# Kernel tuning notes

Measured on AMD Instinct MI355X. Metric: run time of the kernel, lower is better.

## Reference

```python
import jax, jax.numpy as jnp
import numpy as np

N = 50000          # nodes
E = 800000         # edges (before self loops)
IC = 16            # in_channels; pos = x[:, :3]
H = (64, 64, 128, 128)
OUT = 8
INS = (IC, IC + H[0], IC + H[0] + H[1], IC + H[0] + H[1] + H[2])


def _lin_w(k, fi, fo):
    s = 1.0 / np.sqrt(fi)
    return jax.random.uniform(k, (fi, fo), minval=-s, maxval=s, dtype=jnp.float32)


def setup_inputs() -> dict:
    key = jax.random.key(0)
    ks = jax.random.split(key, 64)
    inp = {
        "x": jax.random.normal(ks[0], (N, IC), dtype=jnp.float32),
        "edge_index": jax.random.randint(ks[1], (2, E), 0, N, dtype=jnp.int32),
    }
    ki = 2
    for i, (fi, fo) in enumerate(zip(INS, H), start=1):
        inp[f"Wl{i}"] = _lin_w(ks[ki], fi, fo); ki += 1   # lin (values), no bias
        inp[f"Ws{i}"] = _lin_w(ks[ki], fi, fo); ki += 1   # lin_src, no bias
        inp[f"Wd{i}"] = _lin_w(ks[ki], fi, fo); ki += 1   # lin_dst, no bias
        inp[f"Wp{i}"] = _lin_w(ks[ki], 3, fo); ki += 1    # pos_nn = Linear(3, fo)
        inp[f"bp{i}"] = jnp.zeros((fo,), jnp.float32)
    inp["Wm1"] = _lin_w(ks[ki], IC + sum(H), 64); ki += 1
    inp["bm1"] = jnp.zeros((64,), jnp.float32)
    inp["Wm2"] = _lin_w(ks[ki], 64, OUT); ki += 1
    inp["bm2"] = jnp.zeros((OUT,), jnp.float32)
    return inp


def _pt_conv(h, pos, src, dst, Wl, Ws, Wd, Wp, bp, n):
    """PointTransformerConv: per-channel softmax attention over incoming edges."""
    a_src = h @ Ws                               # alpha_j part  [N, F]
    a_dst = h @ Wd                               # alpha_i part  [N, F]
    v = h @ Wl                                   # values        [N, F]
    delta = (pos[dst] - pos[src]) @ Wp + bp      # pos_nn(pos_i - pos_j)  [E, F]
    alpha = a_dst[dst] - a_src[src] + delta      # [E, F]
    m = jax.ops.segment_max(alpha, dst, num_segments=n)
    ea = jnp.exp(alpha - m[dst])
    s = jax.ops.segment_sum(ea, dst, num_segments=n)
    attn = ea / s[dst]                           # segment softmax (self loops -> s > 0)
    return jax.ops.segment_sum(attn * (v[src] + delta), dst, num_segments=n)


def reference(x, edge_index, Wl1, Ws1, Wd1, Wp1, bp1, Wl2, Ws2, Wd2, Wp2, bp2,
              Wl3, Ws3, Wd3, Wp3, bp3, Wl4, Ws4, Wd4, Wp4, bp4, Wm1, bm1, Wm2, bm2):
    n = x.shape[0]
    pos = x[:, :3]
    loop = jnp.arange(n, dtype=edge_index.dtype)
    src = jnp.concatenate([edge_index[0], loop])  # PyG add_self_loops (default True)
    dst = jnp.concatenate([edge_index[1], loop])
    lrelu = lambda v: jax.nn.leaky_relu(v, 0.01)
    x1 = lrelu(_pt_conv(x, pos, src, dst, Wl1, Ws1, Wd1, Wp1, bp1, n))
    h2 = jnp.concatenate([x, x1], 1)
    x2 = lrelu(_pt_conv(h2, pos, src, dst, Wl2, Ws2, Wd2, Wp2, bp2, n))
    h3 = jnp.concatenate([x, x1, x2], 1)
    x3 = lrelu(_pt_conv(h3, pos, src, dst, Wl3, Ws3, Wd3, Wp3, bp3, n))
    h4 = jnp.concatenate([x, x1, x2, x3], 1)
    x4 = lrelu(_pt_conv(h4, pos, src, dst, Wl4, Ws4, Wd4, Wp4, bp4, n))
    out = jnp.concatenate([x, x1, x2, x3, x4], 1)  # dropout = identity (eval mode)
    out = out @ Wm1 + bm1
    return out @ Wm2 + bm2
```

## Files before the change

kernel.cpp:

```cpp
#include <hip/hip_runtime.h>
#include <hip/hip_bf16.h>
#include <hip/hip_fp16.h>
#include <math.h>

#define N_NODES 50000
#define N_EDGES 800000
#define ET (N_EDGES + N_NODES)
#define HTOT 400

#define SCAN_CHUNK 1024
#define NSCB ((N_NODES + SCAN_CHUNK - 1) / SCAN_CHUNK)

typedef __attribute__((ext_vector_type(4))) float f32x4;
typedef __attribute__((ext_vector_type(8))) short bf16x8;

static const int INS_h[4] = {16, 80, 144, 272};
static const int K32_h[4] = {32, 96, 160, 288};
static const int HO_h[4]  = {64, 64, 128, 128};


__global__ void copy_x_kernel(const float* __restrict__ x, __hip_bfloat16* __restrict__ h) {
    int i = blockIdx.x * blockDim.x + threadIdx.x;
    if (i >= N_NODES * 16) return;
    int n = i >> 4, c = i & 15;
    h[n * HTOT + c] = __float2bfloat16(x[i]);
}

__global__ void hist_kernel(const int* __restrict__ ei, int* __restrict__ deg) {
    int e = blockIdx.x * blockDim.x + threadIdx.x;
    if (e >= ET) return;
    int dst = (e < N_EDGES) ? ei[N_EDGES + e] : (e - N_EDGES);
    atomicAdd(&deg[dst], 1);
}

__global__ __launch_bounds__(256) void scan_p1(const int* __restrict__ deg,
                                               int* __restrict__ bsum) {
    __shared__ int red[256];
    const int b = blockIdx.x, t = threadIdx.x;
    const int base = b * SCAN_CHUNK + t * 4;
    int s = 0;
#pragma unroll
    for (int j = 0; j < 4; ++j) {
        int i = base + j;
        if (i < N_NODES) s += deg[i];
    }
    red[t] = s;
    __syncthreads();
    for (int off = 128; off > 0; off >>= 1) {
        if (t < off) red[t] += red[t + off];
        __syncthreads();
    }
    if (t == 0) bsum[b] = red[0];
}

__global__ void scan_p2(int* __restrict__ bsum) {
    const int lane = threadIdx.x;
    int v = (lane < NSCB) ? bsum[lane] : 0;
    int inc = v;
#pragma unroll
    for (int off = 1; off < 64; off <<= 1) {
        int u = __shfl_up(inc, off);
        if (lane >= off) inc += u;
    }
    if (lane < NSCB) bsum[lane] = inc - v;
    if (lane == 63) bsum[NSCB] = inc;
}

__global__ __launch_bounds__(256) void scan_p3(const int* __restrict__ deg,
                                               const int* __restrict__ bsum,
                                               int* __restrict__ row_ptr,
                                               int* __restrict__ cursor) {
    __shared__ int ts[256];
    const int b = blockIdx.x, t = threadIdx.x;
    const int base = b * SCAN_CHUNK + t * 4;
    int v[4];
    int s = 0;
#pragma unroll
    for (int j = 0; j < 4; ++j) {
        int i = base + j;
        v[j] = (i < N_NODES) ? deg[i] : 0;
        s += v[j];
    }
    ts[t] = s;
    __syncthreads();
    for (int off = 1; off < 256; off <<= 1) {
        int u = (t >= off) ? ts[t - off] : 0;
        __syncthreads();
        ts[t] += u;
        __syncthreads();
    }
    int excl = bsum[b] + ts[t] - s;
#pragma unroll
    for (int j = 0; j < 4; ++j) {
        int i = base + j;
        if (i < N_NODES) {
            row_ptr[i] = excl;
            cursor[i] = excl;
            excl += v[j];
        }
    }
    if (b == 0 && t == 0) row_ptr[N_NODES] = bsum[NSCB];
}

__global__ void scatter_kernel(const int* __restrict__ ei, const float* __restrict__ x,
                               int* __restrict__ cursor, float4* __restrict__ edata) {
    int e = blockIdx.x * blockDim.x + threadIdx.x;
    if (e >= ET) return;
    int src, dst;
    if (e < N_EDGES) { src = ei[e]; dst = ei[N_EDGES + e]; }
    else             { src = dst = e - N_EDGES; }
    int p = atomicAdd(&cursor[dst], 1);
    float dx = x[dst * 16 + 0] - x[src * 16 + 0];
    float dy = x[dst * 16 + 1] - x[src * 16 + 1];
    float dz = x[dst * 16 + 2] - x[src * 16 + 2];
    edata[p] = make_float4(__int_as_float(src), dx, dy, dz);
}


__global__ void concat_wT_kernel(const float* __restrict__ W0, const float* __restrict__ W1,
                                 int K, int K32, int fo,
                                 __hip_bfloat16* __restrict__ Wt, int total) {
    int i = blockIdx.x * blockDim.x + threadIdx.x;
    if (i >= total) return;
    int c = i / K32, kk = i - c * K32;
    float v = 0.f;
    if (kk < K) {
        if (c < fo) v = W0[kk * fo + c];
        else        v = W1[kk * fo + (c - fo)];
    }
    Wt[i] = __float2bfloat16(v);
}


template <bool FUSE>
__global__ __launch_bounds__(256) void gemm3_kernel(
    const __hip_bfloat16* __restrict__ A, int lda,
    const __hip_bfloat16* __restrict__ Wt, int K32,
    const float* __restrict__ bias,
    __half* __restrict__ av, int fo,
    int M, int K,
    const float* __restrict__ W2, const float* __restrict__ b2,
    float* __restrict__ out) {
    __shared__ float smemf[9728];
    ushort* sA = (ushort*)smemf;
    ushort* sB = (ushort*)smemf + 10240;
    const int t = threadIdx.x;
    const int r0 = blockIdx.x * 128, c0 = blockIdx.y * 64;
    const int w = t >> 6, lane = t & 63;
    const int l15 = lane & 15, l4 = lane >> 4;

    f32x4 acc[2][4];
#pragma unroll
    for (int i = 0; i < 2; ++i)
#pragma unroll
        for (int j = 0; j < 4; ++j) acc[i][j] = (f32x4){0.f, 0.f, 0.f, 0.f};

    const int sr = t >> 2, sq = (t & 3) * 8;
    const int ar1 = min(r0 + sr, M - 1), ar2 = min(r0 + sr + 64, M - 1);
    const size_t a1b = (size_t)ar1 * lda, a2b = (size_t)ar2 * lda;
    const size_t wb = (size_t)(c0 + sr) * K32;
    const int nk = K32 >> 5;

    uint4 ga0, ga1, gb;
    const uint4 z4 = {0u, 0u, 0u, 0u};
    {
        const int kk = sq;
        const bool ok = kk < K;
        ga0 = ok ? *(const uint4*)(A + a1b + kk) : z4;
        ga1 = ok ? *(const uint4*)(A + a2b + kk) : z4;
        gb  = *(const uint4*)(Wt + wb + kk);
        *(uint4*)(sA + sr * 40 + sq) = ga0;
        *(uint4*)(sA + (sr + 64) * 40 + sq) = ga1;
        *(uint4*)(sB + sr * 40 + sq) = gb;
    }
    __syncthreads();

    int buf = 0;
    for (int kc = 0; kc < nk; ++kc) {
        const bool nx = (kc + 1) < nk;
        if (nx) {
            const int kk = (kc + 1) * 32 + sq;
            const bool ok = kk < K;
            ga0 = ok ? *(const uint4*)(A + a1b + kk) : z4;
            ga1 = ok ? *(const uint4*)(A + a2b + kk) : z4;
            gb  = *(const uint4*)(Wt + wb + kk);
        }
        const ushort* bA = sA + buf * 5120 + w * 1280;
        const ushort* bB = sB + buf * 2560;
        bf16x8 af[2], bfr[4];
#pragma unroll
        for (int i = 0; i < 2; ++i)
            af[i] = *(const bf16x8*)(bA + (i * 16 + l15) * 40 + l4 * 8);
#pragma unroll
        for (int j = 0; j < 4; ++j)
            bfr[j] = *(const bf16x8*)(bB + (j * 16 + l15) * 40 + l4 * 8);
#pragma unroll
        for (int i = 0; i < 2; ++i)
#pragma unroll
            for (int j = 0; j < 4; ++j)
                acc[i][j] = __builtin_amdgcn_mfma_f32_16x16x32_bf16(af[i], bfr[j], acc[i][j], 0, 0, 0);
        if (nx) {
            const int ob = buf ^ 1;
            *(uint4*)(sA + ob * 5120 + sr * 40 + sq) = ga0;
            *(uint4*)(sA + ob * 5120 + (sr + 64) * 40 + sq) = ga1;
            *(uint4*)(sB + ob * 2560 + sr * 40 + sq) = gb;
        }
        __syncthreads();
        buf ^= 1;
    }

    if (!FUSE) {
#pragma unroll
        for (int i = 0; i < 2; ++i)
#pragma unroll
            for (int j = 0; j < 4; ++j)
#pragma unroll
                for (int p = 0; p < 4; ++p) {
                    int row = r0 + w * 32 + i * 16 + l4 * 4 + p;
                    int col = c0 + j * 16 + l15;
                    if (row < M) {
                        int part = col >= fo;
                        int cc = col - part * fo;
                        av[((size_t)row * fo + cc) * 2 + part] = __float2half(acc[i][j][p]);
                    }
                }
    } else {
#pragma unroll
        for (int i = 0; i < 2; ++i)
#pragma unroll
            for (int j = 0; j < 4; ++j)
#pragma unroll
                for (int p = 0; p < 4; ++p) {
                    int lrow = w * 32 + i * 16 + l4 * 4 + p;
                    int col = j * 16 + l15;
                    smemf[lrow * 68 + col] = acc[i][j][p] + bias[col];
                }
        smemf[8704 + t] = W2[t];
        smemf[8704 + 256 + t] = W2[256 + t];
        __syncthreads();
        const int row = t >> 1, oc = (t & 1) * 4;
        f32x4 o = *(const f32x4*)&b2[oc];
#pragma unroll 8
        for (int k = 0; k < 64; ++k) {
            float a = smemf[row * 68 + k];
            o += a * *(const f32x4*)&smemf[8704 + k * 8 + oc];
        }
        const int grow = r0 + row;
        if (grow < M) *(f32x4*)&out[(size_t)grow * 8 + oc] = o;
    }
}


template <int CPL>
__global__ __launch_bounds__(256) void attn_kernel(
    __hip_bfloat16* __restrict__ h,
    const __half* __restrict__ av,
    const float* __restrict__ Wp, const float* __restrict__ bp,
    const int* __restrict__ rowp, const float4* __restrict__ edata,
    int colbase) {
    constexpr int FO = 16 * CPL;
    constexpr int NV = CPL / 4;
    const int wid = (blockIdx.x * (int)blockDim.x + (int)threadIdx.x) >> 6;
    if (wid >= N_NODES) return;
    const int lane = threadIdx.x & 63;
    const int e = lane >> 4, l16 = lane & 15;
    const int n = wid;
    const int cb = l16 * CPL;

    float wp0[CPL], wp1[CPL], wp2[CPL], bpv[CPL], s[CPL], num[CPL];
#pragma unroll
    for (int j = 0; j < CPL; ++j) {
        int c = cb + j;
        wp0[j] = Wp[c];
        wp1[j] = Wp[FO + c];
        wp2[j] = Wp[2 * FO + c];
        bpv[j] = bp[c];
        s[j] = 0.f; num[j] = 0.f;
    }
    const uint* av32 = (const uint*)av;
    const int beg = rowp[n], end = rowp[n + 1], last = end - 1;

    uint4 u[NV], un[NV];
    float4 ed, edn;
    {
        const int idx = min(beg + e, last);
        ed = edata[idx];
        const uint* rb = av32 + (size_t)__float_as_int(ed.x) * FO + cb;
#pragma unroll
        for (int q = 0; q < NV; ++q) u[q] = *(const uint4*)(rb + 4 * q);
    }
    for (int base = beg; base < end; base += 4) {
        const int nidx = min(base + 4 + e, last);
        edn = edata[nidx];
        const uint* rb = av32 + (size_t)__float_as_int(edn.x) * FO + cb;
#pragma unroll
        for (int q = 0; q < NV; ++q) un[q] = *(const uint4*)(rb + 4 * q);
        const bool val = (base + e) < end;
        const uint* up = (const uint*)u;
#pragma unroll
        for (int j = 0; j < CPL; ++j) {
            __half2 hv = *(const __half2*)&up[j];
            float as = __half2float(hv.x);
            float vv = __half2float(hv.y);
            float delta = fmaf(ed.y, wp0[j], fmaf(ed.z, wp1[j], fmaf(ed.w, wp2[j], bpv[j])));
            float p = val ? __expf(delta - as) : 0.f;
            s[j] += p;
            num[j] = fmaf(p, vv + delta, num[j]);
        }
        ed = edn;
#pragma unroll
        for (int q = 0; q < NV; ++q) u[q] = un[q];
    }
#pragma unroll
    for (int j = 0; j < CPL; ++j) {
        s[j] += __shfl_xor(s[j], 16);
        s[j] += __shfl_xor(s[j], 32);
        num[j] += __shfl_xor(num[j], 16);
        num[j] += __shfl_xor(num[j], 32);
    }
    if (e == 0) {
        ushort o[CPL];
#pragma unroll
        for (int j = 0; j < CPL; ++j) {
            float xi = num[j] / s[j];
            xi = xi > 0.f ? xi : 0.01f * xi;
            __hip_bfloat16 b = __float2bfloat16(xi);
            o[j] = *(ushort*)&b;
        }
        ushort* dst = (ushort*)&h[(size_t)n * HTOT + colbase + cb];
        if (CPL == 4)      *(uint2*)dst = *(uint2*)o;
        else               *(uint4*)dst = *(uint4*)o;
    }
}


extern "C" void kernel_launch(void* const* d_in, const int* in_sizes, int n_in,
                              void* d_out, int out_size, void* d_ws, size_t ws_size,
                              hipStream_t stream) {
    const float* x = (const float*)d_in[0];
    const int* ei = (const int*)d_in[1];
    const float *Wl[4], *Ws[4], *Wp[4], *bp[4];
    for (int i = 0; i < 4; ++i) {
        Wl[i] = (const float*)d_in[2 + 5 * i];
        Ws[i] = (const float*)d_in[3 + 5 * i];
        Wp[i] = (const float*)d_in[5 + 5 * i];
        bp[i] = (const float*)d_in[6 + 5 * i];
    }
    const float* Wm1 = (const float*)d_in[22];
    const float* bm1 = (const float*)d_in[23];
    const float* Wm2 = (const float*)d_in[24];
    const float* bm2 = (const float*)d_in[25];
    float* out = (float*)d_out;

    char* ws = (char*)d_ws;
    size_t off = 0;
    auto alloc = [&](size_t bytes) -> void* {
        void* p = ws + off;
        off += (bytes + 255) & ~(size_t)255;
        return p;
    };
    __hip_bfloat16* h = (__hip_bfloat16*)alloc((size_t)N_NODES * HTOT * 2);
    __half* av = (__half*)alloc((size_t)N_NODES * 256 * 2);
    __hip_bfloat16* Wt = (__hip_bfloat16*)alloc((size_t)384 * 416 * 2);
    int* deg = (int*)alloc((size_t)N_NODES * 4);
    int* rowp = (int*)alloc((size_t)(N_NODES + 1) * 4);
    int* cursor = (int*)alloc((size_t)N_NODES * 4);
    int* bsum = (int*)alloc((size_t)(NSCB + 1) * 4);
    float4* edata = (float4*)alloc((size_t)ET * 16);
    (void)ws_size; (void)n_in; (void)in_sizes; (void)out_size;

    hipMemsetAsync(deg, 0, (size_t)N_NODES * 4, stream);
    copy_x_kernel<<<(N_NODES * 16 + 255) / 256, 256, 0, stream>>>(x, h);
    hist_kernel<<<(ET + 255) / 256, 256, 0, stream>>>(ei, deg);
    scan_p1<<<NSCB, 256, 0, stream>>>(deg, bsum);
    scan_p2<<<1, 64, 0, stream>>>(bsum);
    scan_p3<<<NSCB, 256, 0, stream>>>(deg, bsum, rowp, cursor);
    scatter_kernel<<<(ET + 255) / 256, 256, 0, stream>>>(ei, x, cursor, edata);

    const int M = N_NODES;
    const int gx = (M + 127) / 128;
    const int nbn = (N_NODES + 3) / 4;
    for (int L = 0; L < 4; ++L) {
        const int K = INS_h[L], K32 = K32_h[L], fo = HO_h[L], n2 = 2 * fo;
        const int total = n2 * K32;
        concat_wT_kernel<<<(total + 255) / 256, 256, 0, stream>>>(Ws[L], Wl[L],
                                                                  K, K32, fo, Wt, total);
        dim3 g(gx, n2 / 64);
        gemm3_kernel<false><<<g, 256, 0, stream>>>(h, HTOT, Wt, K32, nullptr, av, fo,
                                                   M, K, nullptr, nullptr, nullptr);
        if (fo == 64)
            attn_kernel<4><<<nbn, 256, 0, stream>>>(h, av, Wp[L], bp[L], rowp, edata, K);
        else
            attn_kernel<8><<<nbn, 256, 0, stream>>>(h, av, Wp[L], bp[L], rowp, edata, K);
    }
    {
        const int total = 64 * 416;
        concat_wT_kernel<<<(total + 255) / 256, 256, 0, stream>>>(Wm1, nullptr,
                                                                  400, 416, 64, Wt, total);
        gemm3_kernel<true><<<dim3(gx, 1), 256, 0, stream>>>(h, HTOT, Wt, 416, bm1,
                                                            nullptr, 0, M, 400, Wm2, bm2, out);
    }
}
```

Before: 401.7 us.

## Fuse prep kernels and use packed half math in attention

Merges the x copy, degree zeroing and all weight transpose/concat launches into one prep kernel, so six launches plus a memset become one. The GEMM now stores the attention-source half pre-scaled by -log2(e) in a planar layout (all scores, then all values) instead of interleaved pairs. The attention kernel computes delta with packed half2 FMAs and uses exp2f. This reduces launch overhead and per-edge ALU work, at the cost of lower precision in the delta computation.

New measurement: 386.9 us. 3.7% less time.

```diff
diff --git a/kernel.cpp b/kernel.cpp
--- a/kernel.cpp
+++ b/kernel.cpp
@@ -18,13 +18,55 @@
 static const int K32_h[4] = {32, 96, 160, 288};
 static const int HO_h[4]  = {64, 64, 128, 128};
 
-
-__global__ void copy_x_kernel(const float* __restrict__ x, __hip_bfloat16* __restrict__ h) {
-    int i = blockIdx.x * blockDim.x + threadIdx.x;
-    if (i >= N_NODES * 16) return;
-    int n = i >> 4, c = i & 15;
-    h[n * HTOT + c] = __float2bfloat16(x[i]);
-}
+#define LOG2E_F 1.4426950408889634f
+
+
+struct PrepArgs {
+    const float* x; __hip_bfloat16* h; int* deg;
+    const float* Ws0; const float* Wl0;
+    const float* Ws1; const float* Wl1;
+    const float* Ws2; const float* Wl2;
+    const float* Ws3; const float* Wl3;
+    const float* Wm1;
+    __hip_bfloat16* Wt0; __hip_bfloat16* Wt1; __hip_bfloat16* Wt2;
+    __hip_bfloat16* Wt3; __hip_bfloat16* WtF;
+};
+
+__device__ inline void concat1(const float* __restrict__ W0, const float* __restrict__ W1,
+                               int K, int K32, int fo, __hip_bfloat16* __restrict__ Wt, int i) {
+    int c = i / K32, kk = i - c * K32;
+    float v = 0.f;
+    if (kk < K) v = (c < fo) ? W0[kk * fo + c] : W1[kk * fo + (c - fo)];
+    Wt[i] = __float2bfloat16(v);
+}
+
+#define PREP_TOTAL 1007696
+
+__global__ __launch_bounds__(256) void prep_kernel(PrepArgs a) {
+    int i = blockIdx.x * 256 + threadIdx.x;
+    if (i < 800000) {
+        int n = i >> 4, c = i & 15;
+        a.h[n * HTOT + c] = __float2bfloat16(a.x[i]);
+        return;
+    }
+    i -= 800000;
+    if (i < 50000) { a.deg[i] = 0; return; }
+    i -= 50000;
+    if (i < 4096)  { concat1(a.Ws0, a.Wl0, 16, 32, 64, a.Wt0, i); return; }
+    i -= 4096;
+    if (i < 12288) { concat1(a.Ws1, a.Wl1, 80, 96, 64, a.Wt1, i); return; }
+    i -= 12288;
+    if (i < 40960) { concat1(a.Ws2, a.Wl2, 144, 160, 128, a.Wt2, i); return; }
+    i -= 40960;
+    if (i < 73728) { concat1(a.Ws3, a.Wl3, 272, 288, 128, a.Wt3, i); return; }
+    i -= 73728;
+    if (i < 26624) {
+        int c = i / 416, kk = i - c * 416;
+        float v = (kk < 400) ? a.Wm1[kk * 64 + c] : 0.f;
+        a.WtF[i] = __float2bfloat16(v);
+    }
+}
+
 
 __global__ void hist_kernel(const int* __restrict__ ei, int* __restrict__ deg) {
     int e = blockIdx.x * blockDim.x + threadIdx.x;
@@ -114,21 +156,6 @@
     float dy = x[dst * 16 + 1] - x[src * 16 + 1];
     float dz = x[dst * 16 + 2] - x[src * 16 + 2];
     edata[p] = make_float4(__int_as_float(src), dx, dy, dz);
-}
-
-
-__global__ void concat_wT_kernel(const float* __restrict__ W0, const float* __restrict__ W1,
-                                 int K, int K32, int fo,
-                                 __hip_bfloat16* __restrict__ Wt, int total) {
-    int i = blockIdx.x * blockDim.x + threadIdx.x;
-    if (i >= total) return;
-    int c = i / K32, kk = i - c * K32;
-    float v = 0.f;
-    if (kk < K) {
-        if (c < fo) v = W0[kk * fo + c];
-        else        v = W1[kk * fo + (c - fo)];
-    }
-    Wt[i] = __float2bfloat16(v);
 }
 
 
@@ -210,6 +237,7 @@
     }
 
     if (!FUSE) {
+        const int n2 = 2 * fo;
 #pragma unroll
         for (int i = 0; i < 2; ++i)
 #pragma unroll
@@ -219,9 +247,9 @@
                     int row = r0 + w * 32 + i * 16 + l4 * 4 + p;
                     int col = c0 + j * 16 + l15;
                     if (row < M) {
-                        int part = col >= fo;
-                        int cc = col - part * fo;
-                        av[((size_t)row * fo + cc) * 2 + part] = __float2half(acc[i][j][p]);
+                        float vv = acc[i][j][p];
+                        if (col < fo) vv *= -LOG2E_F;
+                        av[(size_t)row * n2 + col] = __float2half(vv);
                     }
                 }
     } else {
@@ -259,57 +287,75 @@
     const int* __restrict__ rowp, const float4* __restrict__ edata,
     int colbase) {
     constexpr int FO = 16 * CPL;
-    constexpr int NV = CPL / 4;
+    constexpr int NU = CPL / 2;
     const int wid = (blockIdx.x * (int)blockDim.x + (int)threadIdx.x) >> 6;
     if (wid >= N_NODES) return;
     const int lane = threadIdx.x & 63;
     const int e = lane >> 4, l16 = lane & 15;
     const int n = wid;
     const int cb = l16 * CPL;
-
-    float wp0[CPL], wp1[CPL], wp2[CPL], bpv[CPL], s[CPL], num[CPL];
-#pragma unroll
-    for (int j = 0; j < CPL; ++j) {
-        int c = cb + j;
-        wp0[j] = Wp[c];
-        wp1[j] = Wp[FO + c];
-        wp2[j] = Wp[2 * FO + c];
-        bpv[j] = bp[c];
-        s[j] = 0.f; num[j] = 0.f;
-    }
-    const uint* av32 = (const uint*)av;
+    const int cb2 = cb >> 1;
+
+    __half2 wp0h[NU], wp1h[NU], wp2h[NU], bph[NU];
+#pragma unroll
+    for (int jj = 0; jj < NU; ++jj) {
+        int c = cb + 2 * jj;
+        wp0h[jj] = __floats2half2_rn(Wp[c], Wp[c + 1]);
+        wp1h[jj] = __floats2half2_rn(Wp[FO + c], Wp[FO + c + 1]);
+        wp2h[jj] = __floats2half2_rn(Wp[2 * FO + c], Wp[2 * FO + c + 1]);
+        bph[jj]  = __floats2half2_rn(bp[c], bp[c + 1]);
+    }
+    float s[CPL], num[CPL];
+#pragma unroll
+    for (int j = 0; j < CPL; ++j) { s[j] = 0.f; num[j] = 0.f; }
+
+    const uint* avu = (const uint*)av;
+    const __half2 L2E = __float2half2_rn(LOG2E_F);
     const int beg = rowp[n], end = rowp[n + 1], last = end - 1;
 
-    uint4 u[NV], un[NV];
+    uint as_c[NU], vv_c[NU], as_n[NU], vv_n[NU];
     float4 ed, edn;
-    {
-        const int idx = min(beg + e, last);
-        ed = edata[idx];
-        const uint* rb = av32 + (size_t)__float_as_int(ed.x) * FO + cb;
-#pragma unroll
-        for (int q = 0; q < NV; ++q) u[q] = *(const uint4*)(rb + 4 * q);
-    }
+
+    auto ld = [&](int idx, float4& edo, uint* as, uint* vv) {
+        edo = edata[idx];
+        const uint* rb = avu + (size_t)__float_as_int(edo.x) * FO;
+        if (CPL == 8) {
+            uint4 a = *(const uint4*)(rb + cb2);
+            uint4 v = *(const uint4*)(rb + FO / 2 + cb2);
+            as[0] = a.x; as[1] = a.y; as[2] = a.z; as[3] = a.w;
+            vv[0] = v.x; vv[1] = v.y; vv[2] = v.z; vv[3] = v.w;
+        } else {
+            uint2 a = *(const uint2*)(rb + cb2);
+            uint2 v = *(const uint2*)(rb + FO / 2 + cb2);
+            as[0] = a.x; as[1] = a.y;
+            vv[0] = v.x; vv[1] = v.y;
+        }
+    };
+
+    ld(min(beg + e, last), ed, as_c, vv_c);
     for (int base = beg; base < end; base += 4) {
-        const int nidx = min(base + 4 + e, last);
-        edn = edata[nidx];
-        const uint* rb = av32 + (size_t)__float_as_int(edn.x) * FO + cb;
-#pragma unroll
-        for (int q = 0; q < NV; ++q) un[q] = *(const uint4*)(rb + 4 * q);
+        ld(min(base + 4 + e, last), edn, as_n, vv_n);
         const bool val = (base + e) < end;
-        const uint* up = (const uint*)u;
-#pragma unroll
-        for (int j = 0; j < CPL; ++j) {
-            __half2 hv = *(const __half2*)&up[j];
-            float as = __half2float(hv.x);
-            float vv = __half2float(hv.y);
-            float delta = fmaf(ed.y, wp0[j], fmaf(ed.z, wp1[j], fmaf(ed.w, wp2[j], bpv[j])));
-            float p = val ? __expf(delta - as) : 0.f;
-            s[j] += p;
-            num[j] = fmaf(p, vv + delta, num[j]);
+        __half2 yh = __float2half2_rn(ed.y);
+        __half2 zh = __float2half2_rn(ed.z);
+        __half2 wh = __float2half2_rn(ed.w);
+#pragma unroll
+        for (int jj = 0; jj < NU; ++jj) {
+            __half2 d  = __hfma2(yh, wp0h[jj], __hfma2(zh, wp1h[jj], __hfma2(wh, wp2h[jj], bph[jj])));
+            __half2 a2 = __hfma2(d, L2E, *(const __half2*)&as_c[jj]);
+            __half2 vd = __hadd2(*(const __half2*)&vv_c[jj], d);
+            float pl = exp2f(__half2float(__low2half(a2)));
+            float ph = exp2f(__half2float(__high2half(a2)));
+            pl = val ? pl : 0.f;
+            ph = val ? ph : 0.f;
+            s[2 * jj]     += pl;
+            s[2 * jj + 1] += ph;
+            num[2 * jj]     = fmaf(pl, __half2float(__low2half(vd)),  num[2 * jj]);
+            num[2 * jj + 1] = fmaf(ph, __half2float(__high2half(vd)), num[2 * jj + 1]);
         }
         ed = edn;
 #pragma unroll
-        for (int q = 0; q < NV; ++q) u[q] = un[q];
+        for (int q = 0; q < NU; ++q) { as_c[q] = as_n[q]; vv_c[q] = vv_n[q]; }
     }
 #pragma unroll
     for (int j = 0; j < CPL; ++j) {
@@ -361,7 +407,11 @@
     };
     __hip_bfloat16* h = (__hip_bfloat16*)alloc((size_t)N_NODES * HTOT * 2);
     __half* av = (__half*)alloc((size_t)N_NODES * 256 * 2);
-    __hip_bfloat16* Wt = (__hip_bfloat16*)alloc((size_t)384 * 416 * 2);
+    __hip_bfloat16* Wt0 = (__hip_bfloat16*)alloc((size_t)4096 * 2);
+    __hip_bfloat16* Wt1 = (__hip_bfloat16*)alloc((size_t)12288 * 2);
+    __hip_bfloat16* Wt2 = (__hip_bfloat16*)alloc((size_t)40960 * 2);
+    __hip_bfloat16* Wt3 = (__hip_bfloat16*)alloc((size_t)73728 * 2);
+    __hip_bfloat16* WtF = (__hip_bfloat16*)alloc((size_t)26624 * 2);
     int* deg = (int*)alloc((size_t)N_NODES * 4);
     int* rowp = (int*)alloc((size_t)(N_NODES + 1) * 4);
     int* cursor = (int*)alloc((size_t)N_NODES * 4);
@@ -369,8 +419,16 @@
     float4* edata = (float4*)alloc((size_t)ET * 16);
     (void)ws_size; (void)n_in; (void)in_sizes; (void)out_size;
 
-    hipMemsetAsync(deg, 0, (size_t)N_NODES * 4, stream);
-    copy_x_kernel<<<(N_NODES * 16 + 255) / 256, 256, 0, stream>>>(x, h);
+    PrepArgs pa;
+    pa.x = x; pa.h = h; pa.deg = deg;
+    pa.Ws0 = Ws[0]; pa.Wl0 = Wl[0];
+    pa.Ws1 = Ws[1]; pa.Wl1 = Wl[1];
+    pa.Ws2 = Ws[2]; pa.Wl2 = Wl[2];
+    pa.Ws3 = Ws[3]; pa.Wl3 = Wl[3];
+    pa.Wm1 = Wm1;
+    pa.Wt0 = Wt0; pa.Wt1 = Wt1; pa.Wt2 = Wt2; pa.Wt3 = Wt3; pa.WtF = WtF;
+    prep_kernel<<<(PREP_TOTAL + 255) / 256, 256, 0, stream>>>(pa);
+
     hist_kernel<<<(ET + 255) / 256, 256, 0, stream>>>(ei, deg);
     scan_p1<<<NSCB, 256, 0, stream>>>(deg, bsum);
     scan_p2<<<1, 64, 0, stream>>>(bsum);
@@ -380,24 +438,17 @@
     const int M = N_NODES;
     const int gx = (M + 127) / 128;
     const int nbn = (N_NODES + 3) / 4;
+    __hip_bfloat16* Wts[4] = {Wt0, Wt1, Wt2, Wt3};
     for (int L = 0; L < 4; ++L) {
         const int K = INS_h[L], K32 = K32_h[L], fo = HO_h[L], n2 = 2 * fo;
-        const int total = n2 * K32;
-        concat_wT_kernel<<<(total + 255) / 256, 256, 0, stream>>>(Ws[L], Wl[L],
-                                                                  K, K32, fo, Wt, total);
         dim3 g(gx, n2 / 64);
-        gemm3_kernel<false><<<g, 256, 0, stream>>>(h, HTOT, Wt, K32, nullptr, av, fo,
+        gemm3_kernel<false><<<g, 256, 0, stream>>>(h, HTOT, Wts[L], K32, nullptr, av, fo,
                                                    M, K, nullptr, nullptr, nullptr);
         if (fo == 64)
             attn_kernel<4><<<nbn, 256, 0, stream>>>(h, av, Wp[L], bp[L], rowp, edata, K);
         else
             attn_kernel<8><<<nbn, 256, 0, stream>>>(h, av, Wp[L], bp[L], rowp, edata, K);
     }
-    {
-        const int total = 64 * 416;
-        concat_wT_kernel<<<(total + 255) / 256, 256, 0, stream>>>(Wm1, nullptr,
-                                                                  400, 416, 64, Wt, total);
-        gemm3_kernel<true><<<dim3(gx, 1), 256, 0, stream>>>(h, HTOT, Wt, 416, bm1,
-                                                            nullptr, 0, M, 400, Wm2, bm2, out);
-    }
-}
+    gemm3_kernel<true><<<dim3(gx, 1), 256, 0, stream>>>(h, HTOT, WtF, 416, bm1,
+                                                        nullptr, 0, M, 400, Wm2, bm2, out);
+}
```
